# Optimization experiments

Measured on AMD Instinct MI355X. Metric: run time of the kernel, lower is better.

## Reference

```python
import jax, jax.numpy as jnp
import numpy as np

N, E, DIN, DH, DOUT = 100000, 600000, 128, 128, 64


def _glorot(k, shape):
    lim = float(np.sqrt(6.0 / (shape[0] + shape[1])))
    return jax.random.uniform(k, shape, jnp.float32, -lim, lim)


def setup_inputs() -> dict:
    key = jax.random.key(0)
    ks = jax.random.split(key, 12)
    return {
        "x": jax.random.normal(ks[0], (N, DIN), jnp.float32),
        "src": jax.random.randint(ks[1], (E,), 0, N),
        "dst": jax.random.randint(ks[2], (E,), 0, N),
        # layer 0: NGNN_SAGEConv = SAGEConv(in,hid) + fc(hid,hid) + fc2(hid,hid)
        "w_self0": _glorot(ks[3], (DIN, DH)), "b_self0": jnp.zeros((DH,), jnp.float32),
        "w_neigh0": _glorot(ks[4], (DIN, DH)),
        "fc_w": _glorot(ks[5], (DH, DH)), "fc_b": jnp.zeros((DH,), jnp.float32),
        "fc2_w": _glorot(ks[6], (DH, DH)), "fc2_b": jnp.zeros((DH,), jnp.float32),
        # layer 1: SAGEConv(hid,hid)
        "w_self1": _glorot(ks[7], (DH, DH)), "b_self1": jnp.zeros((DH,), jnp.float32),
        "w_neigh1": _glorot(ks[8], (DH, DH)),
        # layer 2: SAGEConv(hid,out)
        "w_self2": _glorot(ks[9], (DH, DOUT)), "b_self2": jnp.zeros((DOUT,), jnp.float32),
        "w_neigh2": _glorot(ks[10], (DH, DOUT)),
    }


def _sage_conv(x, src, dst, w_self, b_self, w_neigh):
    # DGL SAGEConv, aggregator='mean': out = x @ W_self + b + mean_{u->v} x_u @ W_neigh
    agg = jax.ops.segment_sum(x[src], dst, num_segments=N)          # [N, d_in]
    deg = jax.ops.segment_sum(jnp.ones((src.shape[0],), x.dtype), dst, num_segments=N)
    h_neigh = agg / jnp.maximum(deg, 1.0)[:, None]                  # zero-in-degree -> 0
    return x @ w_self + b_self + h_neigh @ w_neigh


def reference(x, src, dst,
              w_self0, b_self0, w_neigh0, fc_w, fc_b, fc2_w, fc2_b,
              w_self1, b_self1, w_neigh1,
              w_self2, b_self2, w_neigh2):
    # layer 0: NGNN_SAGEConv with num_nonl_layers=2, then outer ReLU (dropout: eval = identity)
    h = _sage_conv(x, src, dst, w_self0, b_self0, w_neigh0)
    h = jax.nn.relu(h)
    h = h @ fc_w + fc_b
    h = jax.nn.relu(h)
    h = h @ fc2_w + fc2_b
    h = jax.nn.relu(h)
    # layer 1: SAGEConv + ReLU
    h = _sage_conv(h, src, dst, w_self1, b_self1, w_neigh1)
    h = jax.nn.relu(h)
    # layer 2 (output): SAGEConv, no activation
    return _sage_conv(h, src, dst, w_self2, b_self2, w_neigh2)
```

## Files before the change

kernel.cpp:

```cpp
#include <hip/hip_runtime.h>

#define N_NODES 100000
#define N_EDGES 600000
#define K_DIM   128
#define NPART   ((N_NODES + 255) / 256)
#define EBLK    ((N_EDGES + 255) / 256)
#define CASTB   (N_NODES * K_DIM / 8 / 256)

typedef unsigned short ushort_t;
typedef short v8s __attribute__((ext_vector_type(8)));
typedef float v4f __attribute__((ext_vector_type(4)));

__device__ __forceinline__ ushort_t f2b(float f) {
  unsigned u = __builtin_bit_cast(unsigned, f);
  unsigned r = u + 0x7FFFu + ((u >> 16) & 1u);
  return (ushort_t)(r >> 16);
}
__device__ __forceinline__ float b2f(ushort_t h) {
  return __builtin_bit_cast(float, (unsigned)h << 16);
}
__device__ __forceinline__ float blo(unsigned u) {
  return __builtin_bit_cast(float, u << 16);
}
__device__ __forceinline__ float bhi(unsigned u) {
  return __builtin_bit_cast(float, u & 0xFFFF0000u);
}
__device__ __forceinline__ unsigned pk2(float lo, float hi) {
  return (unsigned)f2b(lo) | ((unsigned)f2b(hi) << 16);
}


__global__ void deg_cast_kernel(const int* __restrict__ dst, int* __restrict__ deg,
                                const float* __restrict__ X, ushort_t* __restrict__ Xb) {
  if (blockIdx.x < EBLK) {
    int e = blockIdx.x * 256 + threadIdx.x;
    if (e < N_EDGES) atomicAdd(&deg[dst[e]], 1);
  } else {
    int i = ((blockIdx.x - EBLK) * 256 + threadIdx.x) * 8;
    if (i >= N_NODES * K_DIM) return;
    float4 v0 = *(const float4*)(X + i);
    float4 v1 = *(const float4*)(X + i + 4);
    ushort4 h0, h1;
    h0.x = f2b(v0.x); h0.y = f2b(v0.y); h0.z = f2b(v0.z); h0.w = f2b(v0.w);
    h1.x = f2b(v1.x); h1.y = f2b(v1.y); h1.z = f2b(v1.z); h1.w = f2b(v1.w);
    *(ushort4*)(Xb + i)     = h0;
    *(ushort4*)(Xb + i + 4) = h1;
  }
}

__global__ void scan1_swz_kernel(
    const int* __restrict__ deg, int* __restrict__ excl, int* __restrict__ partials,
    const float* __restrict__ w0, const float* __restrict__ w1,
    const float* __restrict__ w2, const float* __restrict__ w3,
    const float* __restrict__ w4, const float* __restrict__ w5,
    const float* __restrict__ w6, const float* __restrict__ w7,
    ushort_t* __restrict__ s0, ushort_t* __restrict__ s1,
    ushort_t* __restrict__ s2, ushort_t* __restrict__ s3,
    ushort_t* __restrict__ s4, ushort_t* __restrict__ s5,
    ushort_t* __restrict__ s6, ushort_t* __restrict__ s7) {
  __shared__ int s[256];
  if (blockIdx.x < NPART) {
    int t = threadIdx.x, i = blockIdx.x * 256 + t;
    int v = (i < N_NODES) ? deg[i] : 0;
    s[t] = v;
    __syncthreads();
    for (int off = 1; off < 256; off <<= 1) {
      int x = (t >= off) ? s[t - off] : 0;
      __syncthreads();
      s[t] += x;
      __syncthreads();
    }
    if (i < N_NODES) excl[i] = s[t] - v;
    if (t == 255) partials[blockIdx.x] = s[t];
  } else {
    const int blk = blockIdx.x - NPART;
    const int z = blk >> 6;
    const float* W;
    ushort_t* S;
    int dout = 128;
    switch (z) {
      case 0: W = w0; S = s0; break;
      case 1: W = w1; S = s1; break;
      case 2: W = w2; S = s2; break;
      case 3: W = w3; S = s3; break;
      case 4: W = w4; S = s4; break;
      case 5: W = w5; S = s5; break;
      case 6: W = w6; S = s6; dout = 64; break;
      default: W = w7; S = s7; dout = 64; break;
    }
    int t = (blk & 63) * 256 + threadIdx.x;
    if (t >= K_DIM * dout) return;
    int k = t / dout, n = t % dout;
    S[(k >> 3) * (dout * 8) + n * 8 + (k & 7)] = f2b(W[t]);
  }
}

__global__ void scan2_kernel(int* __restrict__ partials) {
  __shared__ int s[512];
  int t = threadIdx.x;
  int v = (t < NPART) ? partials[t] : 0;
  s[t] = v;
  __syncthreads();
  for (int off = 1; off < 512; off <<= 1) {
    int x = (t >= off) ? s[t - off] : 0;
    __syncthreads();
    s[t] += x;
    __syncthreads();
  }
  if (t < NPART) partials[t] = s[t] - v;
}

__global__ void scan3_kernel(const int* __restrict__ excl, const int* __restrict__ partials,
                             const int* __restrict__ deg, int* __restrict__ row_ptr,
                             int* __restrict__ cursor, float* __restrict__ inv_deg) {
  int i = blockIdx.x * blockDim.x + threadIdx.x;
  if (i < N_NODES) {
    int rp = excl[i] + partials[i >> 8];
    row_ptr[i] = rp;
    cursor[i] = rp;
    inv_deg[i] = 1.0f / (float)(deg[i] > 1 ? deg[i] : 1);
  } else if (i == N_NODES) {
    row_ptr[N_NODES] = N_EDGES;
  }
}

__global__ void fill_kernel(const int* __restrict__ src, const int* __restrict__ dst,
                            int* __restrict__ cursor, int* __restrict__ ssrc) {
  int e = blockIdx.x * blockDim.x + threadIdx.x;
  if (e < N_EDGES) {
    int p = atomicAdd(&cursor[dst[e]], 1);
    ssrc[p] = src[e];
  }
}


template <int DOUT, bool RELU, bool BF16_OUT>
__global__ __launch_bounds__(512, 4) void sage_layer_kernel(
    const ushort_t* __restrict__ H,
    const ushort_t* __restrict__ Wself_sw, const ushort_t* __restrict__ Wneigh_sw,
    const float* __restrict__ bias,
    const int* __restrict__ row_ptr, const int* __restrict__ ssrc,
    const float* __restrict__ inv_deg,
    ushort_t* __restrict__ Obf, float* __restrict__ Ofp) {
  constexpr int NT  = DOUT / 16;
  constexpr int SWN = K_DIM * DOUT;
  constexpr int NW  = SWN / 4096;
  constexpr int HP  = 136;
  __shared__ ushort_t bufW[SWN];
  __shared__ ushort_t aggb[128 * HP];

  const int tid   = threadIdx.x;
  const int wv    = tid >> 6;
  const int lane  = tid & 63;
  const int lm    = lane & 15;
  const int q     = lane >> 4;
  const int lrow0 = wv * 16;
  const int row0  = blockIdx.x * 128 + lrow0;

  #pragma unroll
  for (int j = 0; j < NW; ++j)
    *(uint4*)&bufW[tid * 8 + j * 4096] = *(const uint4*)&Wself_sw[tid * 8 + j * 4096];
  uint4 wreg[NW];
  #pragma unroll
  for (int j = 0; j < NW; ++j)
    wreg[j] = *(const uint4*)&Wneigh_sw[tid * 8 + j * 4096];
  __syncthreads();

  {
    const int c0 = lm * 8;
    for (int rr = 0; rr < 4; ++rr) {
      const int lr = q * 4 + rr;
      int gv = row0 + lr;
      const int vv = gv < N_NODES ? gv : N_NODES - 1;
      float a[8];
      #pragma unroll
      for (int i = 0; i < 8; ++i) a[i] = 0.f;
      const int beg = row_ptr[vv], end = row_ptr[vv + 1];
      int e = beg;
      for (; e + 4 <= end; e += 4) {
        const int s0 = ssrc[e];
        const int s1 = ssrc[e + 1];
        const int s2 = ssrc[e + 2];
        const int s3 = ssrc[e + 3];
        const uint4 p0 = *(const uint4*)(H + (size_t)s0 * K_DIM + c0);
        const uint4 p1 = *(const uint4*)(H + (size_t)s1 * K_DIM + c0);
        const uint4 p2 = *(const uint4*)(H + (size_t)s2 * K_DIM + c0);
        const uint4 p3 = *(const uint4*)(H + (size_t)s3 * K_DIM + c0);
        a[0] += (blo(p0.x) + blo(p1.x)) + (blo(p2.x) + blo(p3.x));
        a[1] += (bhi(p0.x) + bhi(p1.x)) + (bhi(p2.x) + bhi(p3.x));
        a[2] += (blo(p0.y) + blo(p1.y)) + (blo(p2.y) + blo(p3.y));
        a[3] += (bhi(p0.y) + bhi(p1.y)) + (bhi(p2.y) + bhi(p3.y));
        a[4] += (blo(p0.z) + blo(p1.z)) + (blo(p2.z) + blo(p3.z));
        a[5] += (bhi(p0.z) + bhi(p1.z)) + (bhi(p2.z) + bhi(p3.z));
        a[6] += (blo(p0.w) + blo(p1.w)) + (blo(p2.w) + blo(p3.w));
        a[7] += (bhi(p0.w) + bhi(p1.w)) + (bhi(p2.w) + bhi(p3.w));
      }
      if (e + 2 <= end) {
        const int s0 = ssrc[e];
        const int s1 = ssrc[e + 1];
        const uint4 p0 = *(const uint4*)(H + (size_t)s0 * K_DIM + c0);
        const uint4 p1 = *(const uint4*)(H + (size_t)s1 * K_DIM + c0);
        a[0] += blo(p0.x) + blo(p1.x);
        a[1] += bhi(p0.x) + bhi(p1.x);
        a[2] += blo(p0.y) + blo(p1.y);
        a[3] += bhi(p0.y) + bhi(p1.y);
        a[4] += blo(p0.z) + blo(p1.z);
        a[5] += bhi(p0.z) + bhi(p1.z);
        a[6] += blo(p0.w) + blo(p1.w);
        a[7] += bhi(p0.w) + bhi(p1.w);
        e += 2;
      }
      if (e < end) {
        const int s0 = ssrc[e];
        const uint4 p0 = *(const uint4*)(H + (size_t)s0 * K_DIM + c0);
        a[0] += blo(p0.x);
        a[1] += bhi(p0.x);
        a[2] += blo(p0.y);
        a[3] += bhi(p0.y);
        a[4] += blo(p0.z);
        a[5] += bhi(p0.z);
        a[6] += blo(p0.w);
        a[7] += bhi(p0.w);
      }
      const float sc = inv_deg[vv];
      uint4 ov;
      ov.x = pk2(a[0] * sc, a[1] * sc);
      ov.y = pk2(a[2] * sc, a[3] * sc);
      ov.z = pk2(a[4] * sc, a[5] * sc);
      ov.w = pk2(a[6] * sc, a[7] * sc);
      *(uint4*)&aggb[(lrow0 + lr) * HP + c0] = ov;
    }
  }

  int ra = row0 + lm;  ra = ra < N_NODES ? ra : N_NODES - 1;
  const size_t off0 = (size_t)ra * K_DIM;

  v4f acc[NT];
  #pragma unroll
  for (int n = 0; n < NT; ++n) acc[n] = (v4f){0.f, 0.f, 0.f, 0.f};

  for (int ks = 0; ks < K_DIM / 32; ++ks) {
    const int ko = ks * 32 + q * 8;
    const v8s a0 = *(const v8s*)(H + off0 + ko);
    #pragma unroll
    for (int nt = 0; nt < NT; ++nt) {
      const v8s b = *(const v8s*)&bufW[((ks * 4 + q) * DOUT + nt * 16 + lm) * 8];
      acc[nt] = __builtin_amdgcn_mfma_f32_16x16x32_bf16(a0, b, acc[nt], 0, 0, 0);
    }
  }
  __syncthreads();

  #pragma unroll
  for (int j = 0; j < NW; ++j)
    *(uint4*)&bufW[tid * 8 + j * 4096] = wreg[j];
  __syncthreads();

  for (int ks = 0; ks < K_DIM / 32; ++ks) {
    const int ko = ks * 32 + q * 8;
    const v8s a0 = *(const v8s*)&aggb[(lrow0 + lm) * HP + ko];
    #pragma unroll
    for (int nt = 0; nt < NT; ++nt) {
      const v8s b = *(const v8s*)&bufW[((ks * 4 + q) * DOUT + nt * 16 + lm) * 8];
      acc[nt] = __builtin_amdgcn_mfma_f32_16x16x32_bf16(a0, b, acc[nt], 0, 0, 0);
    }
  }

  #pragma unroll
  for (int nt = 0; nt < NT; ++nt) {
    const int col = nt * 16 + lm;
    const float bv = bias[col];
    #pragma unroll
    for (int r = 0; r < 4; ++r) {
      const int row = row0 + q * 4 + r;
      if (row < N_NODES) {
        float v = acc[nt][r] + bv;
        if (RELU) v = v > 0.f ? v : 0.f;
        if (BF16_OUT) Obf[(size_t)row * DOUT + col] = f2b(v);
        else          Ofp[(size_t)row * DOUT + col] = v;
      }
    }
  }
}


__global__ __launch_bounds__(512, 4) void fused_fc_kernel(
    const ushort_t* __restrict__ A,
    const ushort_t* __restrict__ W1sw, const ushort_t* __restrict__ W2sw,
    const float* __restrict__ b1, const float* __restrict__ b2,
    ushort_t* __restrict__ O) {
  constexpr int NT = 8;
  constexpr int HP = 136;
  __shared__ ushort_t bufW[K_DIM * 128];
  __shared__ ushort_t bufH[128 * HP];

  const int tid   = threadIdx.x;
  const int wv    = tid >> 6;
  const int lane  = tid & 63;
  const int lm    = lane & 15;
  const int q     = lane >> 4;
  const int lrow0 = wv * 16;
  const int row0  = blockIdx.x * 128 + lrow0;

  for (int i = tid * 8; i < K_DIM * 128; i += 4096)
    *(uint4*)&bufW[i] = *(const uint4*)&W1sw[i];

  uint4 wreg[4];
  #pragma unroll
  for (int j = 0; j < 4; ++j)
    wreg[j] = *(const uint4*)&W2sw[tid * 8 + j * 4096];

  __syncthreads();

  int ra = row0 + lm;  ra = ra < N_NODES ? ra : N_NODES - 1;
  const size_t off0 = (size_t)ra * K_DIM;

  v4f acc[NT];
  #pragma unroll
  for (int n = 0; n < NT; ++n) acc[n] = (v4f){0.f, 0.f, 0.f, 0.f};

  for (int ks = 0; ks < K_DIM / 32; ++ks) {
    const int ko = ks * 32 + q * 8;
    const v8s a0 = *(const v8s*)(A + off0 + ko);
    #pragma unroll
    for (int nt = 0; nt < NT; ++nt) {
      const v8s b = *(const v8s*)&bufW[((ks * 4 + q) * 128 + nt * 16 + lm) * 8];
      acc[nt] = __builtin_amdgcn_mfma_f32_16x16x32_bf16(a0, b, acc[nt], 0, 0, 0);
    }
  }
  __syncthreads();

  #pragma unroll
  for (int j = 0; j < 4; ++j)
    *(uint4*)&bufW[tid * 8 + j * 4096] = wreg[j];
  #pragma unroll
  for (int nt = 0; nt < NT; ++nt) {
    const int col = nt * 16 + lm;
    const float bv = b1[col];
    #pragma unroll
    for (int r = 0; r < 4; ++r) {
      float v = acc[nt][r] + bv;
      v = v > 0.f ? v : 0.f;
      bufH[(lrow0 + q * 4 + r) * HP + col] = f2b(v);
      acc[nt][r] = 0.f;
    }
  }
  __syncthreads();

  for (int ks = 0; ks < K_DIM / 32; ++ks) {
    const int ko = ks * 32 + q * 8;
    const v8s a0 = *(const v8s*)&bufH[(lrow0 + lm) * HP + ko];
    #pragma unroll
    for (int nt = 0; nt < NT; ++nt) {
      const v8s b = *(const v8s*)&bufW[((ks * 4 + q) * 128 + nt * 16 + lm) * 8];
      acc[nt] = __builtin_amdgcn_mfma_f32_16x16x32_bf16(a0, b, acc[nt], 0, 0, 0);
    }
  }

  #pragma unroll
  for (int nt = 0; nt < NT; ++nt) {
    const int col = nt * 16 + lm;
    const float bv = b2[col];
    #pragma unroll
    for (int r = 0; r < 4; ++r) {
      const int row = row0 + q * 4 + r;
      if (row < N_NODES) {
        float v = acc[nt][r] + bv;
        v = v > 0.f ? v : 0.f;
        O[(size_t)row * 128 + col] = f2b(v);
      }
    }
  }
}


extern "C" void kernel_launch(void* const* d_in, const int* in_sizes, int n_in,
                              void* d_out, int out_size, void* d_ws, size_t ws_size,
                              hipStream_t stream) {
  const float* x        = (const float*)d_in[0];
  const int*   src      = (const int*)d_in[1];
  const int*   dst      = (const int*)d_in[2];
  const float* w_self0  = (const float*)d_in[3];
  const float* b_self0  = (const float*)d_in[4];
  const float* w_neigh0 = (const float*)d_in[5];
  const float* fc_w     = (const float*)d_in[6];
  const float* fc_b     = (const float*)d_in[7];
  const float* fc2_w    = (const float*)d_in[8];
  const float* fc2_b    = (const float*)d_in[9];
  const float* w_self1  = (const float*)d_in[10];
  const float* b_self1  = (const float*)d_in[11];
  const float* w_neigh1 = (const float*)d_in[12];
  const float* w_self2  = (const float*)d_in[13];
  const float* b_self2  = (const float*)d_in[14];
  const float* w_neigh2 = (const float*)d_in[15];

  char* p = (char*)d_ws;
  auto carve = [&](size_t bytes) {
    void* q = (void*)p;
    p += (bytes + 511) & ~(size_t)511;
    return q;
  };
  const size_t PLANE = (size_t)N_NODES * K_DIM * sizeof(ushort_t);
  ushort_t* X   = (ushort_t*)carve(PLANE);
  ushort_t* Y   = (ushort_t*)carve(PLANE);
  ushort_t* Z   = (ushort_t*)carve(PLANE);
  ushort_t* ws0 = (ushort_t*)carve(K_DIM * 128 * 2);
  ushort_t* wn0 = (ushort_t*)carve(K_DIM * 128 * 2);
  ushort_t* wfc = (ushort_t*)carve(K_DIM * 128 * 2);
  ushort_t* wf2 = (ushort_t*)carve(K_DIM * 128 * 2);
  ushort_t* ws1 = (ushort_t*)carve(K_DIM * 128 * 2);
  ushort_t* wn1 = (ushort_t*)carve(K_DIM * 128 * 2);
  ushort_t* ws2 = (ushort_t*)carve(K_DIM * 64 * 2);
  ushort_t* wn2 = (ushort_t*)carve(K_DIM * 64 * 2);
  int*   ssrc    = (int*)carve((size_t)N_EDGES * 4);
  int*   row_ptr = (int*)carve((size_t)(N_NODES + 1) * 4);
  int*   cursor  = (int*)carve((size_t)N_NODES * 4);
  int*   deg     = (int*)carve((size_t)N_NODES * 4);
  int*   excl    = (int*)carve((size_t)N_NODES * 4);
  int*   parts   = (int*)carve(512 * 4);
  float* inv_deg = (float*)carve((size_t)N_NODES * 4);

  hipMemsetAsync(deg, 0, (size_t)N_NODES * 4, stream);
  deg_cast_kernel<<<EBLK + CASTB, 256, 0, stream>>>(dst, deg, x, X);
  scan1_swz_kernel<<<NPART + 512, 256, 0, stream>>>(
      deg, excl, parts,
      w_self0, w_neigh0, fc_w, fc2_w, w_self1, w_neigh1, w_self2, w_neigh2,
      ws0, wn0, wfc, wf2, ws1, wn1, ws2, wn2);
  scan2_kernel<<<1, 512, 0, stream>>>(parts);
  scan3_kernel<<<((N_NODES + 1) + 255) / 256, 256, 0, stream>>>(excl, parts, deg,
                                                                row_ptr, cursor, inv_deg);
  fill_kernel<<<EBLK, 256, 0, stream>>>(src, dst, cursor, ssrc);

  const int GB = (N_NODES + 127) / 128;

  sage_layer_kernel<128, true, true><<<GB, 512, 0, stream>>>(
      X, ws0, wn0, b_self0, row_ptr, ssrc, inv_deg, Z, nullptr);
  fused_fc_kernel<<<GB, 512, 0, stream>>>(Z, wfc, wf2, fc_b, fc2_b, Y);
  sage_layer_kernel<128, true, true><<<GB, 512, 0, stream>>>(
      Y, ws1, wn1, b_self1, row_ptr, ssrc, inv_deg, Z, nullptr);
  sage_layer_kernel<64, false, false><<<GB, 512, 0, stream>>>(
      Z, ws2, wn2, b_self2, row_ptr, ssrc, inv_deg, nullptr, (float*)d_out);
}
```

Measured before the change: 379.1 us.

## Spill neighbor aggregates to global scratch to shrink LDS and raise occupancy

The per-block aggregated-neighbor tile moves from shared memory into a global scratch buffer, shrinking LDS to a single 32KB buffer and raising launch bounds to 8 blocks per CU. Epilogue outputs are staged through LDS and written back as coalesced 16-byte vector stores. The aim is more concurrent waves to hide gather latency. The cost is an extra global write and read of the aggregate tile per layer, plus extra barriers.

```diff
diff --git a/kernel.cpp b/kernel.cpp
--- a/kernel.cpp
+++ b/kernel.cpp
@@ -6,6 +6,8 @@
 #define NPART   ((N_NODES + 255) / 256)
 #define EBLK    ((N_EDGES + 255) / 256)
 #define CASTB   (N_NODES * K_DIM / 8 / 256)
+#define GBLK    ((N_NODES + 127) / 128)
+#define VROWS   (GBLK * 128)
 
 typedef unsigned short ushort_t;
 typedef short v8s __attribute__((ext_vector_type(8)));
@@ -135,8 +137,9 @@
 
 
 template <int DOUT, bool RELU, bool BF16_OUT>
-__global__ __launch_bounds__(512, 4) void sage_layer_kernel(
+__global__ __launch_bounds__(512, 8) void sage_layer_kernel(
     const ushort_t* __restrict__ H,
+    ushort_t* __restrict__ AGG,
     const ushort_t* __restrict__ Wself_sw, const ushort_t* __restrict__ Wneigh_sw,
     const float* __restrict__ bias,
     const int* __restrict__ row_ptr, const int* __restrict__ ssrc,
@@ -145,9 +148,7 @@
   constexpr int NT  = DOUT / 16;
   constexpr int SWN = K_DIM * DOUT;
   constexpr int NW  = SWN / 4096;
-  constexpr int HP  = 136;
-  __shared__ ushort_t bufW[SWN];
-  __shared__ ushort_t aggb[128 * HP];
+  __shared__ __align__(16) ushort_t buf[16384];
 
   const int tid   = threadIdx.x;
   const int wv    = tid >> 6;
@@ -159,7 +160,7 @@
 
   #pragma unroll
   for (int j = 0; j < NW; ++j)
-    *(uint4*)&bufW[tid * 8 + j * 4096] = *(const uint4*)&Wself_sw[tid * 8 + j * 4096];
+    *(uint4*)&buf[tid * 8 + j * 4096] = *(const uint4*)&Wself_sw[tid * 8 + j * 4096];
   uint4 wreg[NW];
   #pragma unroll
   for (int j = 0; j < NW; ++j)
@@ -170,7 +171,7 @@
     const int c0 = lm * 8;
     for (int rr = 0; rr < 4; ++rr) {
       const int lr = q * 4 + rr;
-      int gv = row0 + lr;
+      const int gv = row0 + lr;
       const int vv = gv < N_NODES ? gv : N_NODES - 1;
       float a[8];
       #pragma unroll
@@ -228,7 +229,7 @@
       ov.y = pk2(a[2] * sc, a[3] * sc);
       ov.z = pk2(a[4] * sc, a[5] * sc);
       ov.w = pk2(a[6] * sc, a[7] * sc);
-      *(uint4*)&aggb[(lrow0 + lr) * HP + c0] = ov;
+      *(uint4*)&AGG[(size_t)gv * K_DIM + c0] = ov;
     }
   }
 
@@ -244,7 +245,7 @@
     const v8s a0 = *(const v8s*)(H + off0 + ko);
     #pragma unroll
     for (int nt = 0; nt < NT; ++nt) {
-      const v8s b = *(const v8s*)&bufW[((ks * 4 + q) * DOUT + nt * 16 + lm) * 8];
+      const v8s b = *(const v8s*)&buf[((ks * 4 + q) * DOUT + nt * 16 + lm) * 8];
       acc[nt] = __builtin_amdgcn_mfma_f32_16x16x32_bf16(a0, b, acc[nt], 0, 0, 0);
     }
   }
@@ -252,32 +253,60 @@
 
   #pragma unroll
   for (int j = 0; j < NW; ++j)
-    *(uint4*)&bufW[tid * 8 + j * 4096] = wreg[j];
-  __syncthreads();
-
+    *(uint4*)&buf[tid * 8 + j * 4096] = wreg[j];
+  __syncthreads();
+
+  const size_t offA = (size_t)(row0 + lm) * K_DIM;
   for (int ks = 0; ks < K_DIM / 32; ++ks) {
     const int ko = ks * 32 + q * 8;
-    const v8s a0 = *(const v8s*)&aggb[(lrow0 + lm) * HP + ko];
-    #pragma unroll
-    for (int nt = 0; nt < NT; ++nt) {
-      const v8s b = *(const v8s*)&bufW[((ks * 4 + q) * DOUT + nt * 16 + lm) * 8];
+    const v8s a0 = *(const v8s*)(AGG + offA + ko);
+    #pragma unroll
+    for (int nt = 0; nt < NT; ++nt) {
+      const v8s b = *(const v8s*)&buf[((ks * 4 + q) * DOUT + nt * 16 + lm) * 8];
       acc[nt] = __builtin_amdgcn_mfma_f32_16x16x32_bf16(a0, b, acc[nt], 0, 0, 0);
     }
   }
-
-  #pragma unroll
-  for (int nt = 0; nt < NT; ++nt) {
-    const int col = nt * 16 + lm;
-    const float bv = bias[col];
-    #pragma unroll
-    for (int r = 0; r < 4; ++r) {
-      const int row = row0 + q * 4 + r;
-      if (row < N_NODES) {
+  __syncthreads();
+
+  const int base = blockIdx.x * 128;
+  if constexpr (BF16_OUT) {
+    #pragma unroll
+    for (int nt = 0; nt < NT; ++nt) {
+      const int col = nt * 16 + lm;
+      const float bv = bias[col];
+      #pragma unroll
+      for (int r = 0; r < 4; ++r) {
         float v = acc[nt][r] + bv;
         if (RELU) v = v > 0.f ? v : 0.f;
-        if (BF16_OUT) Obf[(size_t)row * DOUT + col] = f2b(v);
-        else          Ofp[(size_t)row * DOUT + col] = v;
-      }
+        buf[(lrow0 + q * 4 + r) * DOUT + col] = f2b(v);
+      }
+    }
+    __syncthreads();
+    #pragma unroll
+    for (int i = tid * 8; i < 128 * DOUT; i += 4096) {
+      const int rw = i / DOUT;
+      if (base + rw < N_NODES)
+        *(uint4*)&Obf[(size_t)(base + rw) * DOUT + (i % DOUT)] = *(const uint4*)&buf[i];
+    }
+  } else {
+    float* fb = (float*)buf;
+    #pragma unroll
+    for (int nt = 0; nt < NT; ++nt) {
+      const int col = nt * 16 + lm;
+      const float bv = bias[col];
+      #pragma unroll
+      for (int r = 0; r < 4; ++r) {
+        float v = acc[nt][r] + bv;
+        if (RELU) v = v > 0.f ? v : 0.f;
+        fb[(lrow0 + q * 4 + r) * DOUT + col] = v;
+      }
+    }
+    __syncthreads();
+    #pragma unroll
+    for (int i = tid * 4; i < 128 * DOUT; i += 2048) {
+      const int rw = i / DOUT;
+      if (base + rw < N_NODES)
+        *(float4*)&Ofp[(size_t)(base + rw) * DOUT + (i % DOUT)] = *(const float4*)&fb[i];
     }
   }
 }
@@ -400,9 +429,10 @@
     return q;
   };
   const size_t PLANE = (size_t)N_NODES * K_DIM * sizeof(ushort_t);
-  ushort_t* X   = (ushort_t*)carve(PLANE);
-  ushort_t* Y   = (ushort_t*)carve(PLANE);
-  ushort_t* Z   = (ushort_t*)carve(PLANE);
+  ushort_t* X    = (ushort_t*)carve(PLANE);
+  ushort_t* Y    = (ushort_t*)carve(PLANE);
+  ushort_t* Z    = (ushort_t*)carve(PLANE);
+  ushort_t* AGGs = (ushort_t*)carve((size_t)VROWS * K_DIM * sizeof(ushort_t));
   ushort_t* ws0 = (ushort_t*)carve(K_DIM * 128 * 2);
   ushort_t* wn0 = (ushort_t*)carve(K_DIM * 128 * 2);
   ushort_t* wfc = (ushort_t*)carve(K_DIM * 128 * 2);
@@ -430,13 +460,13 @@
                                                                 row_ptr, cursor, inv_deg);
   fill_kernel<<<EBLK, 256, 0, stream>>>(src, dst, cursor, ssrc);
 
-  const int GB = (N_NODES + 127) / 128;
+  const int GB = GBLK;
 
   sage_layer_kernel<128, true, true><<<GB, 512, 0, stream>>>(
-      X, ws0, wn0, b_self0, row_ptr, ssrc, inv_deg, Z, nullptr);
+      X, AGGs, ws0, wn0, b_self0, row_ptr, ssrc, inv_deg, Z, nullptr);
   fused_fc_kernel<<<GB, 512, 0, stream>>>(Z, wfc, wf2, fc_b, fc2_b, Y);
   sage_layer_kernel<128, true, true><<<GB, 512, 0, stream>>>(
-      Y, ws1, wn1, b_self1, row_ptr, ssrc, inv_deg, Z, nullptr);
+      Y, AGGs, ws1, wn1, b_self1, row_ptr, ssrc, inv_deg, Z, nullptr);
   sage_layer_kernel<64, false, false><<<GB, 512, 0, stream>>>(
-      Z, ws2, wn2, b_self2, row_ptr, ssrc, inv_deg, nullptr, (float*)d_out);
-}
+      Z, AGGs, ws2, wn2, b_self2, row_ptr, ssrc, inv_deg, nullptr, (float*)d_out);
+}
```

Result: faster. 369.6 us (-2.5%).
